# Optimization experiments

Hardware: AMD Instinct MI355X
Metric: run time of the kernel (lower is better)

## Reference

```python
import jax, jax.numpy as jnp
import numpy as np

IN_F = 256
OUT_F = 256
ALPHA = 0.2  # leaky-relu slope
NEG_INF = -9e15


def setup_inputs() -> dict:
    key = jax.random.key(0)
    ks = jax.random.split(key, 8)
    N_e, N_kc = 10000, 2000
    exercise_h = jax.random.normal(ks[0], (N_e, IN_F), dtype=jnp.float32)
    kc_h = jax.random.normal(ks[1], (N_kc, IN_F), dtype=jnp.float32)
    adj = jax.random.randint(ks[2], (N_e, N_kc), 0, 2, dtype=jnp.int32)
    # parameters (kaiming-ish scaling)
    W1 = jax.random.normal(ks[3], (IN_F, OUT_F), dtype=jnp.float32) * np.sqrt(2.0 / IN_F)
    E = jax.random.normal(ks[4], (IN_F, OUT_F), dtype=jnp.float32) * np.sqrt(2.0 / IN_F)
    a = jax.random.normal(ks[5], (2 * OUT_F, 1), dtype=jnp.float32) * np.sqrt(2.0 / (2 * OUT_F))
    rd_w = jax.random.normal(ks[6], (OUT_F, 2 * OUT_F), dtype=jnp.float32) * np.sqrt(2.0 / (2 * OUT_F))
    rd_b = jnp.zeros((OUT_F,), dtype=jnp.float32)
    return {"exercise_h": exercise_h, "kc_h": kc_h, "adj": adj,
            "W1": W1, "E": E, "a": a, "rd_w": rd_w, "rd_b": rd_b}


def reference(exercise_h, kc_h, adj, W1, E, a, rd_w, rd_b):
    kc_Wh = kc_h @ W1            # [N_kc, D]
    ex_Wh = exercise_h @ W1      # [N_e, D]
    # a . concat(ex_Wh_i, kc_Wh_j) == a1.ex_Wh_i + a2.kc_Wh_j  (avoids [N_e,N_kc,2D] tensor)
    a1 = a[:OUT_F, 0]
    a2 = a[OUT_F:, 0]
    e = jax.nn.leaky_relu((ex_Wh @ a1)[:, None] + (kc_Wh @ a2)[None, :], negative_slope=ALPHA)  # [N_e, N_kc]
    logits = jnp.where(adj > 0, e, jnp.float32(NEG_INF))
    attention = jax.nn.softmax(logits, axis=1)
    new_kc = attention @ kc_Wh           # [N_e, D]
    ex_Eh = exercise_h @ E               # [N_e, D]
    feat = jnp.concatenate([new_kc, new_kc * ex_Eh], axis=1)  # [N_e, 2D]
    out = feat @ rd_w.T + rd_b
    return jax.nn.elu(out)
```

## Files before the change

### kernel.cpp

```cpp
#include <hip/hip_runtime.h>

#define N_E 10000
#define N_KC 2000
#define ALPHA 0.2f

typedef __attribute__((ext_vector_type(8))) short short8;
typedef __attribute__((ext_vector_type(4))) float f32x4;

__device__ float g_w1a1[256];
__device__ __align__(16) float g_t[2080];
__device__ unsigned long long g_bm64[N_E * 32];
__device__ __align__(16) unsigned short g_W1T_pk[16 * 8 * 512];
__device__ __align__(16) unsigned short g_ET_pk[16 * 8 * 512];
__device__ __align__(16) unsigned short g_rdw_pk[16 * 16 * 512];
__device__ __align__(16) unsigned short g_kcWh_pk[16 * 64 * 512];

__device__ __forceinline__ unsigned short f2bf(float f) {
  union { float f; unsigned int u; } v; v.f = f;
  unsigned int r = v.u + 0x7FFFu + ((v.u >> 16) & 1u);
  return (unsigned short)(r >> 16);
}

__device__ __forceinline__ void cvt_store4(float4 v, unsigned short* dst) {
  ushort4 o;
  o.x = f2bf(v.x); o.y = f2bf(v.y); o.z = f2bf(v.z); o.w = f2bf(v.w);
  *reinterpret_cast<ushort4*>(dst) = o;
}

__device__ __forceinline__ unsigned long long spread4(unsigned long long x) {
  x &= 0xFFFFull;
  x = (x | (x << 24)) & 0x000000FF000000FFull;
  x = (x | (x << 12)) & 0x000F000F000F000Full;
  x = (x | (x << 6))  & 0x0303030303030303ull;
  x = (x | (x << 3))  & 0x1111111111111111ull;
  return x;
}

__global__ __launch_bounds__(256) void prep_kernel(
    const int* __restrict__ adj, const float* __restrict__ W1,
    const float* __restrict__ E, const float* __restrict__ a,
    const float* __restrict__ rd_w) {
  int b = blockIdx.x, tid = threadIdx.x;
  if (b < 32) {
#pragma unroll
    for (int s2 = 0; s2 < 2; ++s2) {
      int sId = b * 512 + tid + s2 * 256;
      int ct = sId >> 10, rem = sId & 1023;
      int kt = rem >> 6, lane = rem & 63;
      int g = lane >> 4, r = lane & 15;
      const float* src = rd_w + (size_t)(ct * 16 + r) * 512 + kt * 32 + g * 8;
      unsigned short* dst = g_rdw_pk + (size_t)sId * 8;
      cvt_store4(*(const float4*)src, dst);
      cvt_store4(*(const float4*)(src + 4), dst + 4);
    }
  } else if (b < 48) {
#pragma unroll
    for (int s2 = 0; s2 < 2; ++s2) {
      int sId = (b - 32) * 512 + tid + s2 * 256;
      int ct = sId >> 9, rem = sId & 511;
      int kt = rem >> 6, lane = rem & 63;
      int g = lane >> 4, r = lane & 15;
      int col = ct * 16 + r, k = kt * 32 + g * 8;
      unsigned short* dst = g_W1T_pk + (size_t)sId * 8;
      ushort4 o0, o1;
      o0.x = f2bf(W1[(k + 0) * 256 + col]); o0.y = f2bf(W1[(k + 1) * 256 + col]);
      o0.z = f2bf(W1[(k + 2) * 256 + col]); o0.w = f2bf(W1[(k + 3) * 256 + col]);
      o1.x = f2bf(W1[(k + 4) * 256 + col]); o1.y = f2bf(W1[(k + 5) * 256 + col]);
      o1.z = f2bf(W1[(k + 6) * 256 + col]); o1.w = f2bf(W1[(k + 7) * 256 + col]);
      *(ushort4*)dst = o0; *(ushort4*)(dst + 4) = o1;
    }
  } else if (b < 64) {
#pragma unroll
    for (int s2 = 0; s2 < 2; ++s2) {
      int sId = (b - 48) * 512 + tid + s2 * 256;
      int ct = sId >> 9, rem = sId & 511;
      int kt = rem >> 6, lane = rem & 63;
      int g = lane >> 4, r = lane & 15;
      int col = ct * 16 + r, k = kt * 32 + g * 8;
      unsigned short* dst = g_ET_pk + (size_t)sId * 8;
      ushort4 o0, o1;
      o0.x = f2bf(E[(k + 0) * 256 + col]); o0.y = f2bf(E[(k + 1) * 256 + col]);
      o0.z = f2bf(E[(k + 2) * 256 + col]); o0.w = f2bf(E[(k + 3) * 256 + col]);
      o1.x = f2bf(E[(k + 4) * 256 + col]); o1.y = f2bf(E[(k + 5) * 256 + col]);
      o1.z = f2bf(E[(k + 6) * 256 + col]); o1.w = f2bf(E[(k + 7) * 256 + col]);
      *(ushort4*)dst = o0; *(ushort4*)(dst + 4) = o1;
    }
  } else if (b == 64) {
    float acc = 0.f;
    for (int q = 0; q < 64; ++q) {
      float4 wv = *(const float4*)(W1 + (size_t)tid * 256 + q * 4);
      float4 a4 = *(const float4*)(a + q * 4);
      acc += wv.x * a4.x + wv.y * a4.y + wv.z * a4.z + wv.w * a4.w;
    }
    g_w1a1[tid] = acc;
  } else if (b == 65) {
    for (int idx = tid; idx < 16 * 2 * 512; idx += 256) {
      int ct = idx >> 10, rem = idx & 1023;
      int kt = 62 + (rem >> 9), off = rem & 511;
      g_kcWh_pk[((size_t)ct * 64 + kt) * 512 + off] = 0;
    }
    for (int idx = tid; idx < 2080; idx += 256) g_t[idx] = 0.f;
  } else {
    int w = tid >> 6, lane = tid & 63;
    int row = (b - 66) * 4 + w;
    const int* ap = adj + (size_t)row * N_KC;
#pragma unroll
    for (int it = 0; it < 8; ++it) {
      int c0 = it * 256 + lane * 4;
      int4 v = {0, 0, 0, 0};
      if (c0 < N_KC) v = *(const int4*)(ap + c0);
      unsigned long long m0 = __ballot(v.x > 0);
      unsigned long long m1 = __ballot(v.y > 0);
      unsigned long long m2 = __ballot(v.z > 0);
      unsigned long long m3 = __ballot(v.w > 0);
      if (lane < 4) {
        int sh = lane * 16;
        unsigned long long W = spread4(m0 >> sh) | (spread4(m1 >> sh) << 1) |
                               (spread4(m2 >> sh) << 2) | (spread4(m3 >> sh) << 3);
        g_bm64[(size_t)row * 32 + it * 4 + lane] = W;
      }
    }
  }
}

__global__ __launch_bounds__(256) void kc_mfma_kernel(
    const float* __restrict__ kc_h, const float* __restrict__ a) {
  int tid = threadIdx.x, lane = tid & 63, w = tid >> 6;
  int r = lane & 15, g = lane >> 4;
  int j0 = (blockIdx.x >> 2) * 16;
  int ct = (blockIdx.x & 3) * 4 + w;
  f32x4 acc = {0.f, 0.f, 0.f, 0.f};
  for (int kk = 0; kk < 8; ++kk) {
    int k = kk * 32 + g * 8;
    const float* src = kc_h + (size_t)(j0 + r) * 256 + k;
    float4 x0 = *(const float4*)src, x1 = *(const float4*)(src + 4);
    short8 af = {(short)f2bf(x0.x), (short)f2bf(x0.y), (short)f2bf(x0.z),
                 (short)f2bf(x0.w), (short)f2bf(x1.x), (short)f2bf(x1.y),
                 (short)f2bf(x1.z), (short)f2bf(x1.w)};
    short8 bf = *(const short8*)(g_W1T_pk + ((size_t)ct * 8 + kk) * 512 +
                                 lane * 8);
    acc = __builtin_amdgcn_mfma_f32_16x16x32_bf16(af, bf, acc, 0, 0, 0);
  }
  int j = j0 + g * 4;
  int kt = j >> 5, lsub = ((j >> 3) & 3) * 16 + r, sub = (g & 1) * 4;
  ushort4 o;
  o.x = f2bf(acc[0]); o.y = f2bf(acc[1]); o.z = f2bf(acc[2]); o.w = f2bf(acc[3]);
  *reinterpret_cast<ushort4*>(
      g_kcWh_pk + ((size_t)ct * 64 + kt) * 512 + lsub * 8 + sub) = o;
  float a2v = a[256 + ct * 16 + r];
  float tp[4];
#pragma unroll
  for (int q = 0; q < 4; ++q) tp[q] = acc[q] * a2v;
#pragma unroll
  for (int off = 1; off < 16; off <<= 1)
#pragma unroll
    for (int q = 0; q < 4; ++q) tp[q] += __shfl_xor(tp[q], off, 64);
  if (r == 0)
#pragma unroll
    for (int q = 0; q < 4; ++q) atomicAdd(&g_t[j0 + g * 4 + q], tp[q]);
}

#define PSTR 136
#define FST 536
__global__ __launch_bounds__(512, 4) void main_kernel(
    const float* __restrict__ exh, const float* __restrict__ rd_b,
    float* __restrict__ out) {
  __shared__ __align__(16) unsigned char smem[50816];
  __shared__ float ds_part[8][32];
  __shared__ float red32[32];
  float* t_s = (float*)smem;
  unsigned long long* bm_s = (unsigned long long*)(smem + 8320);
  unsigned short* p_s = (unsigned short*)(smem + 17024);
  unsigned short* exh_pk_s = (unsigned short*)(smem + 34432);
  unsigned short* feat_s = (unsigned short*)smem;

  int tid = threadIdx.x, w = tid >> 6, lane = tid & 63;
  int r = lane & 15, g = lane >> 4;
  int i0 = blockIdx.x * 32;
  int mh = w >> 2, kw = w & 3;

  for (int q = tid; q < 520; q += 512)
    ((float4*)t_s)[q] = ((const float4*)g_t)[q];
  for (int q = tid; q < 32 * 32; q += 512) {
    int rr = q >> 5, wd = q & 31;
    int grow = i0 + rr; grow = grow < N_E ? grow : N_E - 1;
    bm_s[rr * 34 + wd] = g_bm64[(size_t)grow * 32 + wd];
  }
  {
    const float* wsrc = g_w1a1 + w * 32 + g * 8;
    float4 w0 = *(const float4*)wsrc, w1 = *(const float4*)(wsrc + 4);
    float sp[2];
#pragma unroll
    for (int m = 0; m < 2; ++m) {
      int row = i0 + m * 16 + r; row = row < N_E ? row : N_E - 1;
      const float* xsrc = exh + (size_t)row * 256 + w * 32 + g * 8;
      float4 x0 = *(const float4*)xsrc, x1 = *(const float4*)(xsrc + 4);
      unsigned short* dst = exh_pk_s + m * 4096 + w * 512 + lane * 8;
      cvt_store4(x0, dst); cvt_store4(x1, dst + 4);
      sp[m] = x0.x * w0.x + x0.y * w0.y + x0.z * w0.z + x0.w * w0.w +
              x1.x * w1.x + x1.y * w1.y + x1.z * w1.z + x1.w * w1.w;
      sp[m] += __shfl_xor(sp[m], 16, 64);
      sp[m] += __shfl_xor(sp[m], 32, 64);
    }
    if (lane < 16) { ds_part[w][lane] = sp[0]; ds_part[w][16 + lane] = sp[1]; }
  }
  __syncthreads();
  if (tid < 32) {
    float sv = 0.f;
#pragma unroll
    for (int ww = 0; ww < 8; ++ww) sv += ds_part[ww][tid];
    red32[tid] = sv;
  }
  __syncthreads();
  float sv = red32[mh * 16 + r];

  f32x4 accP[2][2] = {{{0.f,0.f,0.f,0.f},{0.f,0.f,0.f,0.f}},
                      {{0.f,0.f,0.f,0.f},{0.f,0.f,0.f,0.f}}};
  f32x4 accE[2][2] = {{{0.f,0.f,0.f,0.f},{0.f,0.f,0.f,0.f}},
                      {{0.f,0.f,0.f,0.f},{0.f,0.f,0.f,0.f}}};
  float dsum = 0.f;

  auto gen = [&](int c) {
    int kk = c * 4 + kw;
    int c0 = kk * 32 + g * 8;
    unsigned mb =
        (unsigned)((bm_s[(mh * 16 + r) * 34 + (c0 >> 6)] >> (c0 & 63)) & 0xFFull);
    float4 t0 = *(const float4*)(t_s + c0);
    float4 t1 = *(const float4*)(t_s + c0 + 4);
    float tv[8] = {t0.x, t0.y, t0.z, t0.w, t1.x, t1.y, t1.z, t1.w};
    unsigned ub[8];
#pragma unroll
    for (int j = 0; j < 8; ++j) {
      float x = sv + tv[j];
      float lx = fmaxf(x, ALPHA * x);
      float pv = ((mb >> j) & 1u) ? __expf(lx) : 0.f;
      dsum += pv;
      ub[j] = __float_as_uint(pv) + 0x8000u;
    }
    int4 pk;
    pk.x = (int)((ub[0] >> 16) | (ub[1] & 0xFFFF0000u));
    pk.y = (int)((ub[2] >> 16) | (ub[3] & 0xFFFF0000u));
    pk.z = (int)((ub[4] >> 16) | (ub[5] & 0xFFFF0000u));
    pk.w = (int)((ub[6] >> 16) | (ub[7] & 0xFFFF0000u));
    *(int4*)(p_s + ((size_t)(c & 1) * 32 + mh * 16 + r) * PSTR + kw * 32 +
             g * 8) = pk;
  };

  auto mfma_chunk = [&](int c) {
    const unsigned short* pb = p_s + (size_t)(c & 1) * 32 * PSTR;
    const unsigned short* bb0 =
        g_kcWh_pk + ((size_t)(w * 2 + 0) * 64 + c * 4) * 512 + lane * 8;
    const unsigned short* bb1 =
        g_kcWh_pk + ((size_t)(w * 2 + 1) * 64 + c * 4) * 512 + lane * 8;
    short8 b0 = *(const short8*)bb0;
    short8 b1 = *(const short8*)bb1;
#pragma unroll
    for (int u = 0; u < 4; ++u) {
      short8 a0 = *(const short8*)(pb + (size_t)r * PSTR + u * 32 + g * 8);
      short8 a1 = *(const short8*)(pb + (size_t)(16 + r) * PSTR + u * 32 + g * 8);
      short8 nb0 = b0, nb1 = b1;
      if (u < 3) {
        nb0 = *(const short8*)(bb0 + (u + 1) * 512);
        nb1 = *(const short8*)(bb1 + (u + 1) * 512);
      }
      accP[0][0] = __builtin_amdgcn_mfma_f32_16x16x32_bf16(a0, b0, accP[0][0], 0, 0, 0);
      accP[1][0] = __builtin_amdgcn_mfma_f32_16x16x32_bf16(a1, b0, accP[1][0], 0, 0, 0);
      accP[0][1] = __builtin_amdgcn_mfma_f32_16x16x32_bf16(a0, b1, accP[0][1], 0, 0, 0);
      accP[1][1] = __builtin_amdgcn_mfma_f32_16x16x32_bf16(a1, b1, accP[1][1], 0, 0, 0);
      b0 = nb0; b1 = nb1;
    }
    if ((c & 1) == 0) {
      int ke = c >> 1;
      short8 a0 = *(const short8*)(exh_pk_s + ke * 512 + lane * 8);
      short8 a1 = *(const short8*)(exh_pk_s + 4096 + ke * 512 + lane * 8);
#pragma unroll
      for (int n = 0; n < 2; ++n) {
        short8 be = *(const short8*)(g_ET_pk + ((size_t)(w * 2 + n) * 8 + ke) *
                                                   512 + lane * 8);
        accE[0][n] = __builtin_amdgcn_mfma_f32_16x16x32_bf16(a0, be, accE[0][n], 0, 0, 0);
        accE[1][n] = __builtin_amdgcn_mfma_f32_16x16x32_bf16(a1, be, accE[1][n], 0, 0, 0);
      }
    }
  };

  gen(0);
  __syncthreads();
  for (int c = 1; c < 16; ++c) {
    gen(c);
    mfma_chunk(c - 1);
    __syncthreads();
  }
  mfma_chunk(15);

  dsum += __shfl_xor(dsum, 16, 64);
  dsum += __shfl_xor(dsum, 32, 64);
  if (lane < 16) {
    ds_part[w][mh * 16 + lane] = dsum;
    ds_part[w][(1 - mh) * 16 + lane] = 0.f;
  }
  __syncthreads();
  if (tid < 32) {
    float s = 0.f;
#pragma unroll
    for (int ww = 0; ww < 8; ++ww) s += ds_part[ww][tid];
    red32[tid] = 1.f / fmaxf(s, 1e-30f);
  }
  __syncthreads();

  int c0e = w * 32;
#pragma unroll
  for (int m = 0; m < 2; ++m)
#pragma unroll
    for (int n = 0; n < 2; ++n) {
      int col = c0e + n * 16 + r;
#pragma unroll
      for (int q = 0; q < 4; ++q) {
        int row = m * 16 + g * 4 + q;
        float nk = accP[m][n][q] * red32[row];
        feat_s[(size_t)row * FST + col] = f2bf(nk);
        feat_s[(size_t)row * FST + 256 + col] = f2bf(nk * accE[m][n][q]);
      }
    }
  __syncthreads();

  f32x4 accO[2][2] = {{{0.f,0.f,0.f,0.f},{0.f,0.f,0.f,0.f}},
                      {{0.f,0.f,0.f,0.f},{0.f,0.f,0.f,0.f}}};
#pragma unroll
  for (int kt = 0; kt < 16; ++kt) {
    int k = kt * 32 + g * 8;
    short8 a0 = *(const short8*)(feat_s + (size_t)r * FST + k);
    short8 a1 = *(const short8*)(feat_s + (size_t)(16 + r) * FST + k);
#pragma unroll
    for (int n = 0; n < 2; ++n) {
      short8 bf = *(const short8*)(g_rdw_pk + ((size_t)(w * 2 + n) * 16 + kt) *
                                                  512 + lane * 8);
      accO[0][n] = __builtin_amdgcn_mfma_f32_16x16x32_bf16(a0, bf, accO[0][n], 0, 0, 0);
      accO[1][n] = __builtin_amdgcn_mfma_f32_16x16x32_bf16(a1, bf, accO[1][n], 0, 0, 0);
    }
  }
#pragma unroll
  for (int m = 0; m < 2; ++m) {
    if (i0 + m * 16 >= N_E) continue;
#pragma unroll
    for (int n = 0; n < 2; ++n) {
      int col = c0e + n * 16 + r;
      float bias = rd_b[col];
#pragma unroll
      for (int q = 0; q < 4; ++q) {
        int row = i0 + m * 16 + g * 4 + q;
        float x = accO[m][n][q] + bias;
        float res = x > 0.f ? x : (__expf(x) - 1.f);
        out[(size_t)row * 256 + col] = res;
      }
    }
  }
}

extern "C" void kernel_launch(void* const* d_in, const int* in_sizes, int n_in,
                              void* d_out, int out_size, void* d_ws,
                              size_t ws_size, hipStream_t stream) {
  const float* exh  = (const float*)d_in[0];
  const float* kc_h = (const float*)d_in[1];
  const int*   adj  = (const int*)d_in[2];
  const float* W1   = (const float*)d_in[3];
  const float* E    = (const float*)d_in[4];
  const float* a    = (const float*)d_in[5];
  const float* rd_w = (const float*)d_in[6];
  const float* rd_b = (const float*)d_in[7];
  float* out = (float*)d_out;

  prep_kernel<<<2566, 256, 0, stream>>>(adj, W1, E, a, rd_w);
  kc_mfma_kernel<<<500, 256, 0, stream>>>(kc_h, a);
  main_kernel<<<(N_E + 31) / 32, 512, 0, stream>>>(exh, rd_b, out);
}
```

Measured before the change: 187.3 us.

## Fold kc projection into prep kernel and replace atomics with partial sums

Merges the kc_h@W1 MFMA kernel into the prep kernel as extra blocks, so one launch and the dependency between the two kernels disappear. Those blocks now read and convert W1 columns directly instead of using a prepacked transposed W1. The atomicAdd accumulation of the attention term t is replaced by per-column-group partial arrays that main_kernel sums when it loads them, which also drops the zeroing pass. The cost is strided uncoalesced W1 reads repeated in each MFMA block, plus four extra loads per t element in main_kernel.

After: 184.3 us. No clear change (-1.6%).

```diff
diff --git a/kernel.cpp b/kernel.cpp
--- a/kernel.cpp
+++ b/kernel.cpp
@@ -8,9 +8,8 @@
 typedef __attribute__((ext_vector_type(4))) float f32x4;
 
 __device__ float g_w1a1[256];
-__device__ __align__(16) float g_t[2080];
+__device__ __align__(16) float g_t_part[4][2000];
 __device__ unsigned long long g_bm64[N_E * 32];
-__device__ __align__(16) unsigned short g_W1T_pk[16 * 8 * 512];
 __device__ __align__(16) unsigned short g_ET_pk[16 * 8 * 512];
 __device__ __align__(16) unsigned short g_rdw_pk[16 * 16 * 512];
 __device__ __align__(16) unsigned short g_kcWh_pk[16 * 64 * 512];
@@ -37,9 +36,10 @@
 }
 
 __global__ __launch_bounds__(256) void prep_kernel(
-    const int* __restrict__ adj, const float* __restrict__ W1,
-    const float* __restrict__ E, const float* __restrict__ a,
-    const float* __restrict__ rd_w) {
+    const int* __restrict__ adj, const float* __restrict__ kc_h,
+    const float* __restrict__ W1, const float* __restrict__ E,
+    const float* __restrict__ a, const float* __restrict__ rd_w) {
+  __shared__ float tshare[4][16];
   int b = blockIdx.x, tid = threadIdx.x;
   if (b < 32) {
 #pragma unroll
@@ -57,22 +57,6 @@
 #pragma unroll
     for (int s2 = 0; s2 < 2; ++s2) {
       int sId = (b - 32) * 512 + tid + s2 * 256;
-      int ct = sId >> 9, rem = sId & 511;
-      int kt = rem >> 6, lane = rem & 63;
-      int g = lane >> 4, r = lane & 15;
-      int col = ct * 16 + r, k = kt * 32 + g * 8;
-      unsigned short* dst = g_W1T_pk + (size_t)sId * 8;
-      ushort4 o0, o1;
-      o0.x = f2bf(W1[(k + 0) * 256 + col]); o0.y = f2bf(W1[(k + 1) * 256 + col]);
-      o0.z = f2bf(W1[(k + 2) * 256 + col]); o0.w = f2bf(W1[(k + 3) * 256 + col]);
-      o1.x = f2bf(W1[(k + 4) * 256 + col]); o1.y = f2bf(W1[(k + 5) * 256 + col]);
-      o1.z = f2bf(W1[(k + 6) * 256 + col]); o1.w = f2bf(W1[(k + 7) * 256 + col]);
-      *(ushort4*)dst = o0; *(ushort4*)(dst + 4) = o1;
-    }
-  } else if (b < 64) {
-#pragma unroll
-    for (int s2 = 0; s2 < 2; ++s2) {
-      int sId = (b - 48) * 512 + tid + s2 * 256;
       int ct = sId >> 9, rem = sId & 511;
       int kt = rem >> 6, lane = rem & 63;
       int g = lane >> 4, r = lane & 15;
@@ -85,7 +69,7 @@
       o1.z = f2bf(E[(k + 6) * 256 + col]); o1.w = f2bf(E[(k + 7) * 256 + col]);
       *(ushort4*)dst = o0; *(ushort4*)(dst + 4) = o1;
     }
-  } else if (b == 64) {
+  } else if (b == 48) {
     float acc = 0.f;
     for (int q = 0; q < 64; ++q) {
       float4 wv = *(const float4*)(W1 + (size_t)tid * 256 + q * 4);
@@ -93,16 +77,16 @@
       acc += wv.x * a4.x + wv.y * a4.y + wv.z * a4.z + wv.w * a4.w;
     }
     g_w1a1[tid] = acc;
-  } else if (b == 65) {
+  } else if (b == 49) {
     for (int idx = tid; idx < 16 * 2 * 512; idx += 256) {
       int ct = idx >> 10, rem = idx & 1023;
       int kt = 62 + (rem >> 9), off = rem & 511;
-      g_kcWh_pk[((size_t)ct * 64 + kt) * 512 + off] = 0;
-    }
-    for (int idx = tid; idx < 2080; idx += 256) g_t[idx] = 0.f;
-  } else {
+      if (kt == 63 || off >= 256)
+        g_kcWh_pk[((size_t)ct * 64 + kt) * 512 + off] = 0;
+    }
+  } else if (b < 2550) {
     int w = tid >> 6, lane = tid & 63;
-    int row = (b - 66) * 4 + w;
+    int row = (b - 50) * 4 + w;
     const int* ap = adj + (size_t)row * N_KC;
 #pragma unroll
     for (int it = 0; it < 8; ++it) {
@@ -120,44 +104,54 @@
         g_bm64[(size_t)row * 32 + it * 4 + lane] = W;
       }
     }
-  }
-}
-
-__global__ __launch_bounds__(256) void kc_mfma_kernel(
-    const float* __restrict__ kc_h, const float* __restrict__ a) {
-  int tid = threadIdx.x, lane = tid & 63, w = tid >> 6;
-  int r = lane & 15, g = lane >> 4;
-  int j0 = (blockIdx.x >> 2) * 16;
-  int ct = (blockIdx.x & 3) * 4 + w;
-  f32x4 acc = {0.f, 0.f, 0.f, 0.f};
-  for (int kk = 0; kk < 8; ++kk) {
-    int k = kk * 32 + g * 8;
-    const float* src = kc_h + (size_t)(j0 + r) * 256 + k;
-    float4 x0 = *(const float4*)src, x1 = *(const float4*)(src + 4);
-    short8 af = {(short)f2bf(x0.x), (short)f2bf(x0.y), (short)f2bf(x0.z),
-                 (short)f2bf(x0.w), (short)f2bf(x1.x), (short)f2bf(x1.y),
-                 (short)f2bf(x1.z), (short)f2bf(x1.w)};
-    short8 bf = *(const short8*)(g_W1T_pk + ((size_t)ct * 8 + kk) * 512 +
-                                 lane * 8);
-    acc = __builtin_amdgcn_mfma_f32_16x16x32_bf16(af, bf, acc, 0, 0, 0);
-  }
-  int j = j0 + g * 4;
-  int kt = j >> 5, lsub = ((j >> 3) & 3) * 16 + r, sub = (g & 1) * 4;
-  ushort4 o;
-  o.x = f2bf(acc[0]); o.y = f2bf(acc[1]); o.z = f2bf(acc[2]); o.w = f2bf(acc[3]);
-  *reinterpret_cast<ushort4*>(
-      g_kcWh_pk + ((size_t)ct * 64 + kt) * 512 + lsub * 8 + sub) = o;
-  float a2v = a[256 + ct * 16 + r];
-  float tp[4];
-#pragma unroll
-  for (int q = 0; q < 4; ++q) tp[q] = acc[q] * a2v;
-#pragma unroll
-  for (int off = 1; off < 16; off <<= 1)
-#pragma unroll
-    for (int q = 0; q < 4; ++q) tp[q] += __shfl_xor(tp[q], off, 64);
-  if (r == 0)
-#pragma unroll
-    for (int q = 0; q < 4; ++q) atomicAdd(&g_t[j0 + g * 4 + q], tp[q]);
+  } else {
+    int kb = b - 2550;
+    int lane = tid & 63, w = tid >> 6;
+    int r = lane & 15, g = lane >> 4;
+    int j0 = (kb >> 2) * 16;
+    int ct = (kb & 3) * 4 + w;
+    int col = ct * 16 + r;
+    f32x4 acc = {0.f, 0.f, 0.f, 0.f};
+    for (int kk = 0; kk < 8; ++kk) {
+      int k = kk * 32 + g * 8;
+      const float* src = kc_h + (size_t)(j0 + r) * 256 + k;
+      float4 x0 = *(const float4*)src, x1 = *(const float4*)(src + 4);
+      short8 af = {(short)f2bf(x0.x), (short)f2bf(x0.y), (short)f2bf(x0.z),
+                   (short)f2bf(x0.w), (short)f2bf(x1.x), (short)f2bf(x1.y),
+                   (short)f2bf(x1.z), (short)f2bf(x1.w)};
+      short8 bf = {(short)f2bf(W1[(size_t)(k + 0) * 256 + col]),
+                   (short)f2bf(W1[(size_t)(k + 1) * 256 + col]),
+                   (short)f2bf(W1[(size_t)(k + 2) * 256 + col]),
+                   (short)f2bf(W1[(size_t)(k + 3) * 256 + col]),
+                   (short)f2bf(W1[(size_t)(k + 4) * 256 + col]),
+                   (short)f2bf(W1[(size_t)(k + 5) * 256 + col]),
+                   (short)f2bf(W1[(size_t)(k + 6) * 256 + col]),
+                   (short)f2bf(W1[(size_t)(k + 7) * 256 + col])};
+      acc = __builtin_amdgcn_mfma_f32_16x16x32_bf16(af, bf, acc, 0, 0, 0);
+    }
+    int j = j0 + g * 4;
+    int kt = j >> 5, lsub = ((j >> 3) & 3) * 16 + r, sub = (g & 1) * 4;
+    ushort4 o;
+    o.x = f2bf(acc[0]); o.y = f2bf(acc[1]);
+    o.z = f2bf(acc[2]); o.w = f2bf(acc[3]);
+    *reinterpret_cast<ushort4*>(
+        g_kcWh_pk + ((size_t)ct * 64 + kt) * 512 + lsub * 8 + sub) = o;
+    float a2v = a[256 + ct * 16 + r];
+    float tp[4];
+#pragma unroll
+    for (int q = 0; q < 4; ++q) tp[q] = acc[q] * a2v;
+#pragma unroll
+    for (int off = 1; off < 16; off <<= 1)
+#pragma unroll
+      for (int q = 0; q < 4; ++q) tp[q] += __shfl_xor(tp[q], off, 64);
+    if (r == 0)
+#pragma unroll
+      for (int q = 0; q < 4; ++q) tshare[w][g * 4 + q] = tp[q];
+    __syncthreads();
+    if (tid < 16)
+      g_t_part[kb & 3][j0 + tid] = tshare[0][tid] + tshare[1][tid] +
+                                   tshare[2][tid] + tshare[3][tid];
+  }
 }
 
 #define PSTR 136
@@ -179,8 +173,20 @@
   int i0 = blockIdx.x * 32;
   int mh = w >> 2, kw = w & 3;
 
-  for (int q = tid; q < 520; q += 512)
-    ((float4*)t_s)[q] = ((const float4*)g_t)[q];
+  for (int q = tid; q < 520; q += 512) {
+    float4 v = {0.f, 0.f, 0.f, 0.f};
+    if (q < 500) {
+      float4 p0 = ((const float4*)g_t_part[0])[q];
+      float4 p1 = ((const float4*)g_t_part[1])[q];
+      float4 p2 = ((const float4*)g_t_part[2])[q];
+      float4 p3 = ((const float4*)g_t_part[3])[q];
+      v.x = p0.x + p1.x + p2.x + p3.x;
+      v.y = p0.y + p1.y + p2.y + p3.y;
+      v.z = p0.z + p1.z + p2.z + p3.z;
+      v.w = p0.w + p1.w + p2.w + p3.w;
+    }
+    ((float4*)t_s)[q] = v;
+  }
   for (int q = tid; q < 32 * 32; q += 512) {
     int rr = q >> 5, wd = q & 31;
     int grow = i0 + rr; grow = grow < N_E ? grow : N_E - 1;
@@ -369,7 +375,6 @@
   const float* rd_b = (const float*)d_in[7];
   float* out = (float*)d_out;
 
-  prep_kernel<<<2566, 256, 0, stream>>>(adj, W1, E, a, rd_w);
-  kc_mfma_kernel<<<500, 256, 0, stream>>>(kc_h, a);
+  prep_kernel<<<3050, 256, 0, stream>>>(adj, kc_h, W1, E, a, rd_w);
   main_kernel<<<(N_E + 31) / 32, 512, 0, stream>>>(exh, rd_b, out);
 }
```
